# Optimization experiments

Measured on AMD Instinct MI355X. Metric: run time of the kernel, lower is better.

Reference implementation:

```python
import jax, jax.numpy as jnp
import numpy as np

HEADS = 8
DIM_HEAD = 64
QUERY_DIM = 512
CONTEXT_DIM = 768
INNER = HEADS * DIM_HEAD  # 512
SCALE = DIM_HEAD ** -0.5


def setup_inputs() -> dict:
    key = jax.random.key(0)
    ks = jax.random.split(key, 7)
    B, N, M = 4, 2048, 2048
    x = jax.random.normal(ks[0], (B, N, QUERY_DIM), dtype=jnp.float32)
    context = jax.random.normal(ks[1], (B, M, CONTEXT_DIM), dtype=jnp.float32)
    # torch Linear weights: [out_features, in_features], y = x @ W.T
    s = 0.02
    Wq = jax.random.normal(ks[2], (INNER, QUERY_DIM), dtype=jnp.float32) * s
    Wk = jax.random.normal(ks[3], (INNER, CONTEXT_DIM), dtype=jnp.float32) * s
    Wv = jax.random.normal(ks[4], (INNER, CONTEXT_DIM), dtype=jnp.float32) * s
    Wo = jax.random.normal(ks[5], (QUERY_DIM, INNER), dtype=jnp.float32) * s
    bo = jax.random.normal(ks[6], (QUERY_DIM,), dtype=jnp.float32) * s
    return {"x": x, "context": context, "Wq": Wq, "Wk": Wk, "Wv": Wv, "Wo": Wo, "bo": bo}


def reference(x, context, Wq, Wk, Wv, Wo, bo):
    b, n, _ = x.shape
    m = context.shape[1]
    h, d = HEADS, DIM_HEAD
    # Projections (bias=False for q/k/v)
    q = jnp.einsum('bnc,ec->bne', x, Wq)        # [b, n, inner]
    k = jnp.einsum('bmc,ec->bme', context, Wk)  # [b, m, inner]
    v = jnp.einsum('bmc,ec->bme', context, Wv)
    # Split heads
    q = q.reshape(b, n, h, d)
    k = k.reshape(b, m, h, d)
    v = v.reshape(b, m, h, d)
    # Scores in fp32 (original casts q,k to float), scaled by dim_head**-0.5
    sim = jnp.einsum('bihd,bjhd->bhij', q.astype(jnp.float32), k.astype(jnp.float32)) * SCALE
    attn = jax.nn.softmax(sim, axis=-1).astype(v.dtype)
    out = jnp.einsum('bhij,bjhd->bihd', attn, v).reshape(b, n, h * d)
    # Output projection with bias (dropout=0 -> identity)
    return jnp.einsum('bne,oe->bno', out, Wo) + bo
```

## Files before the change

kernel.cpp:

```cpp
#include <hip/hip_runtime.h>
#include <hip/hip_bf16.h>
#include <math.h>


typedef __bf16 bf16x8 __attribute__((ext_vector_type(8)));
typedef __bf16 bf16x4 __attribute__((ext_vector_type(4)));
typedef float f32x4 __attribute__((ext_vector_type(4)));

#define QSCALE 0.18033688011112042f

#if __has_builtin(__builtin_amdgcn_exp2f)
#define EXP2(x) __builtin_amdgcn_exp2f(x)
#else
#define EXP2(x) exp2f(x)
#endif

__device__ __forceinline__ f32x4 mfma32(bf16x8 a, bf16x8 b, f32x4 c) {
  return __builtin_amdgcn_mfma_f32_16x16x32_bf16(a, b, c, 0, 0, 0);
}

__global__ __launch_bounds__(256) void cast_all(
    const float* __restrict__ x, const float* __restrict__ ctx,
    const float* __restrict__ wq, const float* __restrict__ wk,
    const float* __restrict__ wv, const float* __restrict__ wo,
    __bf16* __restrict__ xb, __bf16* __restrict__ cb,
    __bf16* __restrict__ wqb, __bf16* __restrict__ wkb,
    __bf16* __restrict__ wvb, __bf16* __restrict__ wob) {
  const int B0 = 1048576;
  const int B1 = 2621440;
  const int B2 = 2686976;
  const int B3 = 2785280;
  const int B4 = 2883584;
  const int B5 = 2949120;
  for (int i = blockIdx.x * blockDim.x + threadIdx.x; i < B5;
       i += gridDim.x * blockDim.x) {
    const float* s;
    __bf16* d;
    int off;
    if (i < B0)      { s = x;   d = xb;  off = i; }
    else if (i < B1) { s = ctx; d = cb;  off = i - B0; }
    else if (i < B2) { s = wq;  d = wqb; off = i - B1; }
    else if (i < B3) { s = wk;  d = wkb; off = i - B2; }
    else if (i < B4) { s = wv;  d = wvb; off = i - B3; }
    else             { s = wo;  d = wob; off = i - B4; }
    float4 f = ((const float4*)s)[off];
    union { __bf16 b[4]; ushort4 u; } cv;
    cv.b[0] = (__bf16)f.x; cv.b[1] = (__bf16)f.y;
    cv.b[2] = (__bf16)f.z; cv.b[3] = (__bf16)f.w;
    ((ushort4*)d)[off] = cv.u;
  }
}

template <int MODE>
__device__ __forceinline__ void gemm_body(
    const __bf16* __restrict__ A, const __bf16* __restrict__ W,
    __bf16* __restrict__ Cout, int Kd, float scale, int m0, int n0,
    __bf16 (*As)[72], __bf16 (*Bs)[72]) {
  const int t = threadIdx.x;
  const int w = t >> 6;
  const int lane = t & 63;
  const int ln = lane & 15;
  const int qd = lane >> 4;
  const int wm = (w >> 1) * 64;
  const int wn = (w & 1) * 64;

  f32x4 zero4 = {0.f, 0.f, 0.f, 0.f};
  f32x4 acc[4][4];
#pragma unroll
  for (int i = 0; i < 4; ++i)
#pragma unroll
    for (int j = 0; j < 4; ++j) acc[i][j] = zero4;

  const int r0 = t >> 2;
  const int c0 = (t & 3) * 16;
  const __bf16* gA0 = A + (size_t)(m0 + r0) * Kd + c0;
  const __bf16* gA1 = A + (size_t)(m0 + r0 + 64) * Kd + c0;
  const __bf16* gB0 = W + (size_t)(n0 + r0) * Kd + c0;
  const __bf16* gB1 = W + (size_t)(n0 + r0 + 64) * Kd + c0;

  uint4 a00 = *(const uint4*)gA0, a01 = *(const uint4*)(gA0 + 8);
  uint4 a10 = *(const uint4*)gA1, a11 = *(const uint4*)(gA1 + 8);
  uint4 b00 = *(const uint4*)gB0, b01 = *(const uint4*)(gB0 + 8);
  uint4 b10 = *(const uint4*)gB1, b11 = *(const uint4*)(gB1 + 8);

  for (int kc = 0; kc < Kd; kc += 64) {
    __syncthreads();
    *(uint4*)&As[r0][c0] = a00;       *(uint4*)&As[r0][c0 + 8] = a01;
    *(uint4*)&As[r0 + 64][c0] = a10;  *(uint4*)&As[r0 + 64][c0 + 8] = a11;
    *(uint4*)&Bs[r0][c0] = b00;       *(uint4*)&Bs[r0][c0 + 8] = b01;
    *(uint4*)&Bs[r0 + 64][c0] = b10;  *(uint4*)&Bs[r0 + 64][c0 + 8] = b11;
    __syncthreads();
    if (kc + 64 < Kd) {
      a00 = *(const uint4*)(gA0 + kc + 64);
      a01 = *(const uint4*)(gA0 + kc + 72);
      a10 = *(const uint4*)(gA1 + kc + 64);
      a11 = *(const uint4*)(gA1 + kc + 72);
      b00 = *(const uint4*)(gB0 + kc + 64);
      b01 = *(const uint4*)(gB0 + kc + 72);
      b10 = *(const uint4*)(gB1 + kc + 64);
      b11 = *(const uint4*)(gB1 + kc + 72);
    }
#pragma unroll
    for (int kst = 0; kst < 2; ++kst) {
      bf16x8 af[4], bfr[4];
#pragma unroll
      for (int i = 0; i < 4; ++i) {
        af[i] = *(const bf16x8*)&As[wm + i * 16 + ln][kst * 32 + qd * 8];
        bfr[i] = *(const bf16x8*)&Bs[wn + i * 16 + ln][kst * 32 + qd * 8];
      }
#pragma unroll
      for (int i = 0; i < 4; ++i)
#pragma unroll
        for (int j = 0; j < 4; ++j) {
          if (MODE == 1)
            acc[i][j] = mfma32(af[i], bfr[j], acc[i][j]);
          else
            acc[i][j] = mfma32(bfr[j], af[i], acc[i][j]);
        }
    }
  }

#pragma unroll
  for (int i = 0; i < 4; ++i)
#pragma unroll
    for (int j = 0; j < 4; ++j) {
      if (MODE == 0) {
        const int gm = m0 + wm + i * 16 + ln;
        const int gn0 = n0 + wn + j * 16 + qd * 4;
        const int bb = gm >> 11, tok = gm & 2047;
        const int hh = gn0 >> 6, dd0 = gn0 & 63;
        bf16x4 v;
#pragma unroll
        for (int rg = 0; rg < 4; ++rg) v[rg] = (__bf16)(acc[i][j][rg] * scale);
        *(bf16x4*)(Cout + (((size_t)bb * 8 + hh) * 2048 + tok) * 64 + dd0) = v;
      } else {
        const int gm0 = m0 + wm + i * 16 + qd * 4;
        const int gn = n0 + wn + j * 16 + ln;
        const int bb = gm0 >> 11, tok0 = gm0 & 2047;
        const int hh = gn >> 6, dd = gn & 63;
        bf16x4 v;
#pragma unroll
        for (int rg = 0; rg < 4; ++rg) v[rg] = (__bf16)acc[i][j][rg];
        *(bf16x4*)(Cout + (((size_t)bb * 8 + hh) * 64 + dd) * 2048 + tok0) = v;
      }
    }
}

__global__ __launch_bounds__(256, 3) void proj_qkv(
    const __bf16* __restrict__ xb, const __bf16* __restrict__ cb,
    const __bf16* __restrict__ Wq, const __bf16* __restrict__ Wk,
    const __bf16* __restrict__ Wv, __bf16* __restrict__ Qw,
    __bf16* __restrict__ Kw, __bf16* __restrict__ Vtw) {
  __shared__ __align__(16) __bf16 As[128][72];
  __shared__ __align__(16) __bf16 Bs[128][72];
  const int m0 = blockIdx.x * 128;
  const int job = blockIdx.y >> 2;
  const int n0 = (blockIdx.y & 3) * 128;
  if (job == 0)
    gemm_body<0>(xb, Wq, Qw, 512, QSCALE, m0, n0, As, Bs);
  else if (job == 1)
    gemm_body<0>(cb, Wk, Kw, 768, 1.0f, m0, n0, As, Bs);
  else
    gemm_body<1>(cb, Wv, Vtw, 768, 1.0f, m0, n0, As, Bs);
}

__global__ __launch_bounds__(256) void gemm_out(
    const __bf16* __restrict__ O0, const __bf16* __restrict__ O1,
    const float* __restrict__ lbuf,
    const __bf16* __restrict__ B,
    float* __restrict__ C, const float* __restrict__ bias) {
  const int m0 = blockIdx.x * 64;
  const int n0 = blockIdx.y * 128;
  const int t = threadIdx.x;
  const int w = t >> 6;
  const int lane = t & 63;
  const int ln = lane & 15;
  const int qd = lane >> 4;
  const int wm = (w >> 1) * 32;
  const int wn = (w & 1) * 64;

  __shared__ __align__(16) __bf16 As[64][72];
  __shared__ __align__(16) __bf16 Bs[128][72];

  f32x4 zero4 = {0.f, 0.f, 0.f, 0.f};
  f32x4 acc[2][4];
#pragma unroll
  for (int i = 0; i < 2; ++i)
#pragma unroll
    for (int j = 0; j < 4; ++j) acc[i][j] = zero4;

  const int r0 = t >> 2;
  const int c0 = (t & 3) * 16;
  const int gm_s = m0 + r0;
  const int bidx = gm_s >> 11, tok_s = gm_s & 2047;
  const size_t aoff = (size_t)gm_s * 512 + c0;
  const __bf16* gB0 = B + (size_t)(n0 + r0) * 512 + c0;
  const __bf16* gB1 = B + (size_t)(n0 + r0 + 64) * 512 + c0;

  float inv[8];
#pragma unroll
  for (int hh = 0; hh < 8; ++hh) {
    const float l0 = lbuf[((size_t)bidx * 8 + hh) * 2048 + tok_s];
    const float l1 = lbuf[65536 + ((size_t)bidx * 8 + hh) * 2048 + tok_s];
    inv[hh] = 1.0f / (l0 + l1);
  }

  uint4 o00 = *(const uint4*)(O0 + aoff), o01 = *(const uint4*)(O0 + aoff + 8);
  uint4 o10 = *(const uint4*)(O1 + aoff), o11 = *(const uint4*)(O1 + aoff + 8);
  uint4 b00 = *(const uint4*)gB0, b01 = *(const uint4*)(gB0 + 8);
  uint4 b10 = *(const uint4*)gB1, b11 = *(const uint4*)(gB1 + 8);

  for (int kc = 0; kc < 512; kc += 64) {
    const float iv = inv[kc >> 6];
    union { bf16x8 v; uint4 u; } u0, u1, r0v, r1v;
    u0.u = o00; u1.u = o10;
#pragma unroll
    for (int e = 0; e < 8; ++e)
      r0v.v[e] = (__bf16)(((float)u0.v[e] + (float)u1.v[e]) * iv);
    u0.u = o01; u1.u = o11;
#pragma unroll
    for (int e = 0; e < 8; ++e)
      r1v.v[e] = (__bf16)(((float)u0.v[e] + (float)u1.v[e]) * iv);
    __syncthreads();
    *(uint4*)&As[r0][c0] = r0v.u;
    *(uint4*)&As[r0][c0 + 8] = r1v.u;
    *(uint4*)&Bs[r0][c0] = b00;       *(uint4*)&Bs[r0][c0 + 8] = b01;
    *(uint4*)&Bs[r0 + 64][c0] = b10;  *(uint4*)&Bs[r0 + 64][c0 + 8] = b11;
    __syncthreads();
    if (kc + 64 < 512) {
      o00 = *(const uint4*)(O0 + aoff + kc + 64);
      o01 = *(const uint4*)(O0 + aoff + kc + 72);
      o10 = *(const uint4*)(O1 + aoff + kc + 64);
      o11 = *(const uint4*)(O1 + aoff + kc + 72);
      b00 = *(const uint4*)(gB0 + kc + 64);
      b01 = *(const uint4*)(gB0 + kc + 72);
      b10 = *(const uint4*)(gB1 + kc + 64);
      b11 = *(const uint4*)(gB1 + kc + 72);
    }
#pragma unroll
    for (int kst = 0; kst < 2; ++kst) {
      bf16x8 af[2], bfr[4];
#pragma unroll
      for (int i = 0; i < 2; ++i)
        af[i] = *(const bf16x8*)&As[wm + i * 16 + ln][kst * 32 + qd * 8];
#pragma unroll
      for (int j = 0; j < 4; ++j)
        bfr[j] = *(const bf16x8*)&Bs[wn + j * 16 + ln][kst * 32 + qd * 8];
#pragma unroll
      for (int i = 0; i < 2; ++i)
#pragma unroll
        for (int j = 0; j < 4; ++j)
          acc[i][j] = mfma32(bfr[j], af[i], acc[i][j]);
    }
  }

#pragma unroll
  for (int i = 0; i < 2; ++i)
#pragma unroll
    for (int j = 0; j < 4; ++j) {
      const int gm = m0 + wm + i * 16 + ln;
      const int gn0 = n0 + wn + j * 16 + qd * 4;
      f32x4 bi = *(const f32x4*)&bias[gn0];
      f32x4 v = acc[i][j] + bi;
      *(f32x4*)&C[(size_t)gm * 512 + gn0] = v;
    }
}

__global__ __launch_bounds__(512, 4) void attn_kernel(
    const __bf16* __restrict__ Q,
    const __bf16* __restrict__ K,
    const __bf16* __restrict__ Vt,
    __bf16* __restrict__ Oh,
    float* __restrict__ lbuf) {
  const int S = 2048;
  const int qt = blockIdx.x;
  const int bh = blockIdx.y;
  const int sp = blockIdx.z;
  const int b = bh >> 3, h = bh & 7;
  const int t = threadIdx.x;
  const int w = t >> 6;
  const int lane = t & 63;
  const int ln = lane & 15;
  const int qd = lane >> 4;

  __shared__ __align__(16) __bf16 Ks[2][128][72];
  __shared__ __align__(16) __bf16 Vs[2][64][136];

  bf16x8 bq[2][2];
  {
    const __bf16* qb =
        Q + ((size_t)bh * S + qt * 256 + w * 32 + ln) * 64 + qd * 8;
#pragma unroll
    for (int mt = 0; mt < 2; ++mt)
#pragma unroll
      for (int kst = 0; kst < 2; ++kst)
        bq[mt][kst] = *(const bf16x8*)(qb + mt * 1024 + kst * 32);
  }

  f32x4 zero4 = {0.f, 0.f, 0.f, 0.f};
  f32x4 o[2][4];
  f32x4 o_l[2];
#pragma unroll
  for (int mt = 0; mt < 2; ++mt) {
#pragma unroll
    for (int i = 0; i < 4; ++i) o[mt][i] = zero4;
    o_l[mt] = zero4;
  }
  bf16x8 ones8;
  {
    union { unsigned short u[8]; bf16x8 v; } U;
#pragma unroll
    for (int e = 0; e < 8; ++e) U.u[e] = 0x3F80;
    ones8 = U.v;
  }

  const int kr = t >> 2, kc0 = (t & 3) * 16;
  const int krow =
      (kr & ~31) | ((kr & 4) << 2) | (((kr >> 3) & 3) << 2) | (kr & 3);
  const int vd = t >> 3, vtok0 = (t & 7) * 16;
  const int kt0 = sp * 8;

  const __bf16* gKbase = K + ((size_t)bh * S + kt0 * 128 + kr) * 64 + kc0;
  const __bf16* gVbase = Vt + ((size_t)bh * 64 + vd) * S + kt0 * 128 + vtok0;

  {
    uint4 kv0 = ((const uint4*)gKbase)[0], kv1 = ((const uint4*)gKbase)[1];
    uint4 vv0 = ((const uint4*)gVbase)[0], vv1 = ((const uint4*)gVbase)[1];
    uint4* dK = (uint4*)&Ks[0][krow][kc0];
    dK[0] = kv0; dK[1] = kv1;
    uint4* dV = (uint4*)&Vs[0][vd][vtok0];
    dV[0] = vv0; dV[1] = vv1;
  }
  uint4 kv0 = ((const uint4*)(gKbase + 8192))[0];
  uint4 kv1 = ((const uint4*)(gKbase + 8192))[1];
  uint4 vv0 = ((const uint4*)(gVbase + 128))[0];
  uint4 vv1 = ((const uint4*)(gVbase + 128))[1];
  __syncthreads();

  int p = 0;
  for (int it = 0; it < 8; ++it) {
    if (it + 1 < 8) {
      uint4* dK = (uint4*)&Ks[p ^ 1][krow][kc0];
      dK[0] = kv0; dK[1] = kv1;
      uint4* dV = (uint4*)&Vs[p ^ 1][vd][vtok0];
      dV[0] = vv0; dV[1] = vv1;
      if (it + 2 < 8) {
        const uint4* gK = (const uint4*)(gKbase + (size_t)(it + 2) * 8192);
        const uint4* gV = (const uint4*)(gVbase + (size_t)(it + 2) * 128);
        kv0 = gK[0]; kv1 = gK[1];
        vv0 = gV[0]; vv1 = gV[1];
      }
    }

    const __bf16 (*Ksp)[72] = Ks[p];
    const __bf16 (*Vsp)[136] = Vs[p];

#pragma unroll
    for (int c = 0; c < 4; ++c) {
      f32x4 s[2][2];
      s[0][0] = zero4; s[0][1] = zero4; s[1][0] = zero4; s[1][1] = zero4;
      __builtin_amdgcn_s_setprio(1);
#pragma unroll
      for (int e = 0; e < 2; ++e) {
        const int nt = c * 2 + e;
#pragma unroll
        for (int kst = 0; kst < 2; ++kst) {
          bf16x8 ak = *(const bf16x8*)&Ksp[nt * 16 + ln][kst * 32 + qd * 8];
          s[e][0] = mfma32(ak, bq[0][kst], s[e][0]);
          s[e][1] = mfma32(ak, bq[1][kst], s[e][1]);
        }
      }
      __builtin_amdgcn_s_setprio(0);
#pragma unroll
      for (int e = 0; e < 2; ++e)
#pragma unroll
        for (int mt = 0; mt < 2; ++mt)
#pragma unroll
          for (int rg = 0; rg < 4; ++rg) s[e][mt][rg] = EXP2(s[e][mt][rg]);
      bf16x8 p2[2];
#pragma unroll
      for (int mt = 0; mt < 2; ++mt) {
#pragma unroll
        for (int rg = 0; rg < 4; ++rg) {
          p2[mt][rg] = (__bf16)s[0][mt][rg];
          p2[mt][rg + 4] = (__bf16)s[1][mt][rg];
        }
      }
      __builtin_amdgcn_s_setprio(1);
      o_l[0] = mfma32(ones8, p2[0], o_l[0]);
      o_l[1] = mfma32(ones8, p2[1], o_l[1]);
#pragma unroll
      for (int i = 0; i < 4; ++i) {
        bf16x8 av = *(const bf16x8*)&Vsp[i * 16 + ln][c * 32 + qd * 8];
        o[0][i] = mfma32(av, p2[0], o[0][i]);
        o[1][i] = mfma32(av, p2[1], o[1][i]);
      }
      __builtin_amdgcn_s_setprio(0);
    }

    __syncthreads();
    p ^= 1;
  }

  __bf16* Osp = Oh + (size_t)sp * 8192 * 512;
#pragma unroll
  for (int mt = 0; mt < 2; ++mt) {
    const int tok = qt * 256 + w * 32 + mt * 16 + ln;
    if (qd == 0) lbuf[((size_t)sp * 32 + bh) * 2048 + tok] = o_l[mt][0];
#pragma unroll
    for (int i = 0; i < 4; ++i) {
      bf16x4 v;
#pragma unroll
      for (int rg = 0; rg < 4; ++rg) v[rg] = (__bf16)o[mt][i][rg];
      const int col = h * 64 + i * 16 + qd * 4;
      *(bf16x4*)&Osp[((size_t)b * S + tok) * 512 + col] = v;
    }
  }
}

extern "C" void kernel_launch(void* const* d_in, const int* in_sizes, int n_in,
                              void* d_out, int out_size, void* d_ws,
                              size_t ws_size, hipStream_t stream) {
  const float* x = (const float*)d_in[0];
  const float* ctx = (const float*)d_in[1];
  const float* Wq = (const float*)d_in[2];
  const float* Wk = (const float*)d_in[3];
  const float* Wv = (const float*)d_in[4];
  const float* Wo = (const float*)d_in[5];
  const float* bo = (const float*)d_in[6];

  char* p = (char*)d_ws;
  __bf16* xb = (__bf16*)p;   p += (size_t)8192 * 512 * 2;
  __bf16* cb = (__bf16*)p;   p += (size_t)8192 * 768 * 2;
  __bf16* wqb = (__bf16*)p;  p += (size_t)512 * 512 * 2;
  __bf16* wkb = (__bf16*)p;  p += (size_t)512 * 768 * 2;
  __bf16* wvb = (__bf16*)p;  p += (size_t)512 * 768 * 2;
  __bf16* wob = (__bf16*)p;  p += (size_t)512 * 512 * 2;
  __bf16* Qw = (__bf16*)p;   p += (size_t)8192 * 512 * 2;
  __bf16* Kw = (__bf16*)p;   p += (size_t)8192 * 512 * 2;
  __bf16* Vtw = (__bf16*)p;  p += (size_t)8192 * 512 * 2;
  __bf16* Oh = (__bf16*)p;   p += (size_t)2 * 8192 * 512 * 2;
  float* lbuf = (float*)p;   p += (size_t)2 * 32 * 2048 * 4;

  cast_all<<<2880, 256, 0, stream>>>(x, ctx, Wq, Wk, Wv, Wo, xb, cb, wqb, wkb,
                                     wvb, wob);

  dim3 gp(64, 12);
  proj_qkv<<<gp, 256, 0, stream>>>(xb, cb, wqb, wkb, wvb, Qw, Kw, Vtw);

  dim3 ga(8, 32, 2);
  attn_kernel<<<ga, 512, 0, stream>>>(Qw, Kw, Vtw, Oh, lbuf);

  dim3 go(128, 4);
  gemm_out<<<go, 256, 0, stream>>>(Oh, Oh + (size_t)8192 * 512, lbuf, wob,
                                   (float*)d_out, bo);
}
```

Measured before the change: 174.7 us.

## Halve attention block to 256 threads with 64 query rows per wave

Shrinks the attention block from 8 waves to 4, so each wave now handles 64 query rows (four 16-row tiles) instead of 32. Each K/V fragment read from shared memory is reused across four query tiles, which cuts LDS reads per MFMA. Each thread now loads twice as many K/V elements into shared memory per stage, and the loop is restructured to hoist K/V fragment loads ahead of a per-tile QK, exp and PV sequence. The cost is more accumulator registers per thread and fewer waves per block to hide latency.

```diff
diff --git a/kernel.cpp b/kernel.cpp
--- a/kernel.cpp
+++ b/kernel.cpp
@@ -266,7 +266,7 @@
     }
 }
 
-__global__ __launch_bounds__(512, 4) void attn_kernel(
+__global__ __launch_bounds__(256, 2) void attn_kernel(
     const __bf16* __restrict__ Q,
     const __bf16* __restrict__ K,
     const __bf16* __restrict__ Vt,
@@ -286,22 +286,22 @@
   __shared__ __align__(16) __bf16 Ks[2][128][72];
   __shared__ __align__(16) __bf16 Vs[2][64][136];
 
-  bf16x8 bq[2][2];
+  bf16x8 bq[4][2];
   {
     const __bf16* qb =
-        Q + ((size_t)bh * S + qt * 256 + w * 32 + ln) * 64 + qd * 8;
-#pragma unroll
-    for (int mt = 0; mt < 2; ++mt)
+        Q + ((size_t)bh * S + qt * 256 + w * 64 + ln) * 64 + qd * 8;
+#pragma unroll
+    for (int mt = 0; mt < 4; ++mt)
 #pragma unroll
       for (int kst = 0; kst < 2; ++kst)
         bq[mt][kst] = *(const bf16x8*)(qb + mt * 1024 + kst * 32);
   }
 
   f32x4 zero4 = {0.f, 0.f, 0.f, 0.f};
-  f32x4 o[2][4];
-  f32x4 o_l[2];
-#pragma unroll
-  for (int mt = 0; mt < 2; ++mt) {
+  f32x4 o[4][4];
+  f32x4 o_l[4];
+#pragma unroll
+  for (int mt = 0; mt < 4; ++mt) {
 #pragma unroll
     for (int i = 0; i < 4; ++i) o[mt][i] = zero4;
     o_l[mt] = zero4;
@@ -320,35 +320,51 @@
   const int vd = t >> 3, vtok0 = (t & 7) * 16;
   const int kt0 = sp * 8;
 
-  const __bf16* gKbase = K + ((size_t)bh * S + kt0 * 128 + kr) * 64 + kc0;
-  const __bf16* gVbase = Vt + ((size_t)bh * 64 + vd) * S + kt0 * 128 + vtok0;
+  const __bf16* gK0 = K + ((size_t)bh * S + kt0 * 128 + kr) * 64 + kc0;
+  const __bf16* gK1 = gK0 + 4096;
+  const __bf16* gV0 = Vt + ((size_t)bh * 64 + vd) * S + kt0 * 128 + vtok0;
+  const __bf16* gV1 = gV0 + 65536;
 
   {
-    uint4 kv0 = ((const uint4*)gKbase)[0], kv1 = ((const uint4*)gKbase)[1];
-    uint4 vv0 = ((const uint4*)gVbase)[0], vv1 = ((const uint4*)gVbase)[1];
-    uint4* dK = (uint4*)&Ks[0][krow][kc0];
-    dK[0] = kv0; dK[1] = kv1;
-    uint4* dV = (uint4*)&Vs[0][vd][vtok0];
-    dV[0] = vv0; dV[1] = vv1;
-  }
-  uint4 kv0 = ((const uint4*)(gKbase + 8192))[0];
-  uint4 kv1 = ((const uint4*)(gKbase + 8192))[1];
-  uint4 vv0 = ((const uint4*)(gVbase + 128))[0];
-  uint4 vv1 = ((const uint4*)(gVbase + 128))[1];
+    uint4 k00 = ((const uint4*)gK0)[0], k01 = ((const uint4*)gK0)[1];
+    uint4 k10 = ((const uint4*)gK1)[0], k11 = ((const uint4*)gK1)[1];
+    uint4 v00 = ((const uint4*)gV0)[0], v01 = ((const uint4*)gV0)[1];
+    uint4 v10 = ((const uint4*)gV1)[0], v11 = ((const uint4*)gV1)[1];
+    uint4* dK0 = (uint4*)&Ks[0][krow][kc0];      dK0[0] = k00; dK0[1] = k01;
+    uint4* dK1 = (uint4*)&Ks[0][krow + 64][kc0]; dK1[0] = k10; dK1[1] = k11;
+    uint4* dV0 = (uint4*)&Vs[0][vd][vtok0];      dV0[0] = v00; dV0[1] = v01;
+    uint4* dV1 = (uint4*)&Vs[0][vd + 32][vtok0]; dV1[0] = v10; dV1[1] = v11;
+  }
+  uint4 pk00 = ((const uint4*)(gK0 + 8192))[0];
+  uint4 pk01 = ((const uint4*)(gK0 + 8192))[1];
+  uint4 pk10 = ((const uint4*)(gK1 + 8192))[0];
+  uint4 pk11 = ((const uint4*)(gK1 + 8192))[1];
+  uint4 pv00 = ((const uint4*)(gV0 + 128))[0];
+  uint4 pv01 = ((const uint4*)(gV0 + 128))[1];
+  uint4 pv10 = ((const uint4*)(gV1 + 128))[0];
+  uint4 pv11 = ((const uint4*)(gV1 + 128))[1];
   __syncthreads();
 
   int p = 0;
   for (int it = 0; it < 8; ++it) {
     if (it + 1 < 8) {
-      uint4* dK = (uint4*)&Ks[p ^ 1][krow][kc0];
-      dK[0] = kv0; dK[1] = kv1;
-      uint4* dV = (uint4*)&Vs[p ^ 1][vd][vtok0];
-      dV[0] = vv0; dV[1] = vv1;
+      uint4* dK0 = (uint4*)&Ks[p ^ 1][krow][kc0];
+      dK0[0] = pk00; dK0[1] = pk01;
+      uint4* dK1 = (uint4*)&Ks[p ^ 1][krow + 64][kc0];
+      dK1[0] = pk10; dK1[1] = pk11;
+      uint4* dV0 = (uint4*)&Vs[p ^ 1][vd][vtok0];
+      dV0[0] = pv00; dV0[1] = pv01;
+      uint4* dV1 = (uint4*)&Vs[p ^ 1][vd + 32][vtok0];
+      dV1[0] = pv10; dV1[1] = pv11;
       if (it + 2 < 8) {
-        const uint4* gK = (const uint4*)(gKbase + (size_t)(it + 2) * 8192);
-        const uint4* gV = (const uint4*)(gVbase + (size_t)(it + 2) * 128);
-        kv0 = gK[0]; kv1 = gK[1];
-        vv0 = gV[0]; vv1 = gV[1];
+        const __bf16* nK0 = gK0 + (size_t)(it + 2) * 8192;
+        const __bf16* nK1 = gK1 + (size_t)(it + 2) * 8192;
+        const __bf16* nV0 = gV0 + (size_t)(it + 2) * 128;
+        const __bf16* nV1 = gV1 + (size_t)(it + 2) * 128;
+        pk00 = ((const uint4*)nK0)[0]; pk01 = ((const uint4*)nK0)[1];
+        pk10 = ((const uint4*)nK1)[0]; pk11 = ((const uint4*)nK1)[1];
+        pv00 = ((const uint4*)nV0)[0]; pv01 = ((const uint4*)nV0)[1];
+        pv10 = ((const uint4*)nV1)[0]; pv11 = ((const uint4*)nV1)[1];
       }
     }
 
@@ -357,45 +373,46 @@
 
 #pragma unroll
     for (int c = 0; c < 4; ++c) {
-      f32x4 s[2][2];
-      s[0][0] = zero4; s[0][1] = zero4; s[1][0] = zero4; s[1][1] = zero4;
-      __builtin_amdgcn_s_setprio(1);
-#pragma unroll
-      for (int e = 0; e < 2; ++e) {
-        const int nt = c * 2 + e;
+      bf16x8 ak[2][2];
+#pragma unroll
+      for (int e = 0; e < 2; ++e)
+#pragma unroll
+        for (int kst = 0; kst < 2; ++kst)
+          ak[e][kst] =
+              *(const bf16x8*)&Ksp[(c * 2 + e) * 16 + ln][kst * 32 + qd * 8];
+      bf16x8 av[4];
+#pragma unroll
+      for (int i = 0; i < 4; ++i)
+        av[i] = *(const bf16x8*)&Vsp[i * 16 + ln][c * 32 + qd * 8];
+
+#pragma unroll
+      for (int mt = 0; mt < 4; ++mt) {
+        f32x4 s0 = zero4, s1 = zero4;
+        __builtin_amdgcn_s_setprio(1);
 #pragma unroll
         for (int kst = 0; kst < 2; ++kst) {
-          bf16x8 ak = *(const bf16x8*)&Ksp[nt * 16 + ln][kst * 32 + qd * 8];
-          s[e][0] = mfma32(ak, bq[0][kst], s[e][0]);
-          s[e][1] = mfma32(ak, bq[1][kst], s[e][1]);
+          s0 = mfma32(ak[0][kst], bq[mt][kst], s0);
+          s1 = mfma32(ak[1][kst], bq[mt][kst], s1);
         }
+        __builtin_amdgcn_s_setprio(0);
+#pragma unroll
+        for (int rg = 0; rg < 4; ++rg) {
+          s0[rg] = EXP2(s0[rg]);
+          s1[rg] = EXP2(s1[rg]);
+        }
+        bf16x8 p2;
+#pragma unroll
+        for (int rg = 0; rg < 4; ++rg) {
+          p2[rg] = (__bf16)s0[rg];
+          p2[rg + 4] = (__bf16)s1[rg];
+        }
+        __builtin_amdgcn_s_setprio(1);
+        o_l[mt] = mfma32(ones8, p2, o_l[mt]);
+#pragma unroll
+        for (int i = 0; i < 4; ++i)
+          o[mt][i] = mfma32(av[i], p2, o[mt][i]);
+        __builtin_amdgcn_s_setprio(0);
       }
-      __builtin_amdgcn_s_setprio(0);
-#pragma unroll
-      for (int e = 0; e < 2; ++e)
-#pragma unroll
-        for (int mt = 0; mt < 2; ++mt)
-#pragma unroll
-          for (int rg = 0; rg < 4; ++rg) s[e][mt][rg] = EXP2(s[e][mt][rg]);
-      bf16x8 p2[2];
-#pragma unroll
-      for (int mt = 0; mt < 2; ++mt) {
-#pragma unroll
-        for (int rg = 0; rg < 4; ++rg) {
-          p2[mt][rg] = (__bf16)s[0][mt][rg];
-          p2[mt][rg + 4] = (__bf16)s[1][mt][rg];
-        }
-      }
-      __builtin_amdgcn_s_setprio(1);
-      o_l[0] = mfma32(ones8, p2[0], o_l[0]);
-      o_l[1] = mfma32(ones8, p2[1], o_l[1]);
-#pragma unroll
-      for (int i = 0; i < 4; ++i) {
-        bf16x8 av = *(const bf16x8*)&Vsp[i * 16 + ln][c * 32 + qd * 8];
-        o[0][i] = mfma32(av, p2[0], o[0][i]);
-        o[1][i] = mfma32(av, p2[1], o[1][i]);
-      }
-      __builtin_amdgcn_s_setprio(0);
     }
 
     __syncthreads();
@@ -404,8 +421,8 @@
 
   __bf16* Osp = Oh + (size_t)sp * 8192 * 512;
 #pragma unroll
-  for (int mt = 0; mt < 2; ++mt) {
-    const int tok = qt * 256 + w * 32 + mt * 16 + ln;
+  for (int mt = 0; mt < 4; ++mt) {
+    const int tok = qt * 256 + w * 64 + mt * 16 + ln;
     if (qd == 0) lbuf[((size_t)sp * 32 + bh) * 2048 + tok] = o_l[mt][0];
 #pragma unroll
     for (int i = 0; i < 4; ++i) {
@@ -449,7 +466,7 @@
   proj_qkv<<<gp, 256, 0, stream>>>(xb, cb, wqb, wkb, wvb, Qw, Kw, Vtw);
 
   dim3 ga(8, 32, 2);
-  attn_kernel<<<ga, 512, 0, stream>>>(Qw, Kw, Vtw, Oh, lbuf);
+  attn_kernel<<<ga, 256, 0, stream>>>(Qw, Kw, Vtw, Oh, lbuf);
 
   dim3 go(128, 4);
   gemm_out<<<go, 256, 0, stream>>>(Oh, Oh + (size_t)8192 * 512, lbuf, wob,
```

After: 172.8 us, median of 2. About the same (-1.1%).
